# Kernel tuning notes

Hardware: AMD Instinct MI355X
Metric: run time of the kernel (lower is better)

## Reference

```python
import jax, jax.numpy as jnp
import numpy as np

N_NODES = 10000
N_GRAPHS = 64
NEG_SLOPE = 0.2
EPS = 1e-16


def gat_conv(x, src, dst, W, a_src, a_dst, bias, heads, out_ch, num_nodes):
    """PyG GATConv (shared lin, add_self_loops already applied to src/dst)."""
    xl = (x @ W).reshape(num_nodes, heads, out_ch)          # [N,H,C]
    alpha_s = jnp.einsum('nhc,hc->nh', xl, a_src)           # [N,H]
    alpha_d = jnp.einsum('nhc,hc->nh', xl, a_dst)           # [N,H]
    e = jax.nn.leaky_relu(alpha_s[src] + alpha_d[dst], NEG_SLOPE)  # [E,H]
    # segment softmax over incoming edges of each destination node
    emax = jax.ops.segment_max(e, dst, num_segments=num_nodes)
    emax = jnp.where(jnp.isfinite(emax), emax, 0.0)
    ee = jnp.exp(e - emax[dst])
    denom = jax.ops.segment_sum(ee, dst, num_segments=num_nodes)
    alpha = ee / (denom[dst] + EPS)                         # [E,H]
    msg = xl[src] * alpha[:, :, None]                       # [E,H,C]
    out = jax.ops.segment_sum(msg, dst, num_segments=num_nodes)  # [N,H,C]
    return out.reshape(num_nodes, heads * out_ch) + bias


def setup_inputs() -> dict:
    key = jax.random.key(0)
    ks = jax.random.split(key, 16)
    H, C, IN = 8, 128, 128
    x = jax.random.normal(ks[0], (N_NODES, IN), jnp.float32)
    edge_index = jax.random.randint(ks[1], (2, 320000), 0, N_NODES, jnp.int64)
    batch = jnp.sort(jax.random.randint(ks[2], (N_NODES,), 0, N_GRAPHS, jnp.int64))
    g = lambda k, shp, fan: jax.random.normal(k, shp, jnp.float32) * (1.0 / np.sqrt(fan))
    return {
        'x': x, 'edge_index': edge_index, 'batch': batch,
        'W1': g(ks[3], (IN, H * C), IN),
        'a_src1': g(ks[4], (H, C), C), 'a_dst1': g(ks[5], (H, C), C),
        'b1': jnp.zeros((H * C,), jnp.float32),
        'W2': g(ks[6], (H * C, C), H * C),
        'a_src2': g(ks[7], (1, C), C), 'a_dst2': g(ks[8], (1, C), C),
        'b2': jnp.zeros((C,), jnp.float32),
        'lin1_w': g(ks[9], (C, 128), C), 'lin1_b': jnp.zeros((128,), jnp.float32),
        'lin2_w': g(ks[10], (128, 1), 128), 'lin2_b': jnp.zeros((1,), jnp.float32),
    }


def reference(x, edge_index, batch, W1, a_src1, a_dst1, b1, W2, a_src2, a_dst2, b2,
              lin1_w, lin1_b, lin2_w, lin2_b):
    loops = jnp.arange(N_NODES, dtype=edge_index.dtype)
    src = jnp.concatenate([edge_index[0], loops])
    dst = jnp.concatenate([edge_index[1], loops])
    h = jax.nn.elu(gat_conv(x, src, dst, W1, a_src1, a_dst1, b1, 8, 128, N_NODES))
    h = jax.nn.elu(gat_conv(h, src, dst, W2, a_src2, a_dst2, b2, 1, 128, N_NODES))
    # global mean pool over graphs
    sums = jax.ops.segment_sum(h, batch, num_segments=N_GRAPHS)
    cnts = jax.ops.segment_sum(jnp.ones((N_NODES,), h.dtype), batch, num_segments=N_GRAPHS)
    pooled = sums / jnp.maximum(cnts, 1.0)[:, None]         # [G,128]
    z = jax.nn.relu(pooled @ lin1_w + lin1_b)
    return (z @ lin2_w + lin2_b).squeeze(1)                 # [G]
```

## Files before the change

### kernel.cpp

```cpp
#include <hip/hip_runtime.h>
#include <math.h>

#define N_NODES 10000
#define N_GRAPHS 64
#define E_RAW 320000
#define E_ALL (E_RAW + N_NODES)
#define NEG_SLOPE 0.2f
#define EPS 1e-16f
#define CAP 192

typedef unsigned short ushort_t;
typedef short short8 __attribute__((ext_vector_type(8)));
typedef float floatx4 __attribute__((ext_vector_type(4)));

static __device__ __forceinline__ float bfl(unsigned u) {
  union { unsigned u; float f; } v; v.u = u << 16; return v.f;
}
static __device__ __forceinline__ float bfh(unsigned u) {
  union { unsigned u; float f; } v; v.u = u & 0xFFFF0000u; return v.f;
}
static __device__ __forceinline__ ushort_t f2bf(float f) {
  union { float f; unsigned u; } v; v.f = f;
  unsigned r = v.u + 0x7FFFu + ((v.u >> 16) & 1u);
  return (ushort_t)(r >> 16);
}

static __device__ __forceinline__ void load16_lds(const ushort_t* gp, ushort_t* ldsbase, int lane) {
#if __has_builtin(__builtin_amdgcn_global_load_lds)
  __builtin_amdgcn_global_load_lds((const __attribute__((address_space(1))) void*)gp,
                                   (__attribute__((address_space(3))) void*)ldsbase, 16, 0, 0);
#else
  *(uint4*)(ldsbase + lane * 8) = *(const uint4*)gp;
#endif
}

static __device__ __forceinline__ void swz_one(const float* __restrict__ W,
                                               ushort_t* __restrict__ Wsw,
                                               int idx, int K, int N) {
  int NT = N >> 4;
  int lane = idx & 63, tile = idx >> 6;
  int nt = tile % NT, kt = tile / NT;
  int n = nt * 16 + (lane & 15);
  int kb = kt * 32 + (lane >> 4) * 8;
  ushort4 lo, hi;
  lo.x = f2bf(W[(size_t)(kb + 0) * N + n]); lo.y = f2bf(W[(size_t)(kb + 1) * N + n]);
  lo.z = f2bf(W[(size_t)(kb + 2) * N + n]); lo.w = f2bf(W[(size_t)(kb + 3) * N + n]);
  hi.x = f2bf(W[(size_t)(kb + 4) * N + n]); hi.y = f2bf(W[(size_t)(kb + 5) * N + n]);
  hi.z = f2bf(W[(size_t)(kb + 6) * N + n]); hi.w = f2bf(W[(size_t)(kb + 7) * N + n]);
  *(ushort4*)(Wsw + (size_t)idx * 8) = lo;
  *(ushort4*)(Wsw + (size_t)idx * 8 + 4) = hi;
}

__global__ __launch_bounds__(1024) void prep_k(const float* __restrict__ x,
                                               const int* __restrict__ batch,
                                               const float* __restrict__ W1,
                                               const float* __restrict__ W2,
                                               ushort_t* __restrict__ xb,
                                               ushort_t* __restrict__ W1sw,
                                               ushort_t* __restrict__ W2sw,
                                               float* __restrict__ zero0,
                                               int* __restrict__ poolcnt) {
  __shared__ int shm[N_GRAPHS];
  const int b = blockIdx.x, t = threadIdx.x;
  if (b < 49) {
    int i4 = b * 1024 + t;
    if (i4 < 49548) *(float4*)(zero0 + i4 * 4) = make_float4(0.f, 0.f, 0.f, 0.f);
  } else if (b == 49) {
    if (t < N_GRAPHS) shm[t] = 0;
    __syncthreads();
    for (int n = t; n < N_NODES; n += 1024) atomicAdd(&shm[batch[n]], 1);
    __syncthreads();
    if (t < N_GRAPHS) poolcnt[t] = shm[t];
  } else if (b < 363) {
    int i4 = (b - 50) * 1024 + t;
    if (i4 < 320000) {
      float4 v = *(const float4*)(x + (size_t)i4 * 4);
      ushort4 o;
      o.x = f2bf(v.x); o.y = f2bf(v.y); o.z = f2bf(v.z); o.w = f2bf(v.w);
      *(ushort4*)(xb + (size_t)i4 * 4) = o;
    }
  } else if (b < 379) {
    int idx = (b - 363) * 1024 + t;
    if (idx < 16384) swz_one(W1, W1sw, idx, 128, 1024);
  } else {
    int idx = (b - 379) * 1024 + t;
    if (idx < 16384) swz_one(W2, W2sw, idx, 1024, 128);
  }
}

__global__ __launch_bounds__(256) void g1f_k(const ushort_t* __restrict__ A,
                                             const ushort_t* __restrict__ Bsw,
                                             ushort_t* __restrict__ Cb,
                                             const float* __restrict__ aS,
                                             const float* __restrict__ aD,
                                             float* __restrict__ asO,
                                             float* __restrict__ adO,
                                             const int* __restrict__ ei,
                                             int* __restrict__ degc,
                                             int* __restrict__ csr) {
  __shared__ ushort_t Albuf[32 * 512];
  __shared__ float epi[4][16][68];
  const int bid = blockIdx.x, t = threadIdx.x;
  if (bid >= 632) {
    int e = (bid - 632) * 256 + t;
    if (e < E_ALL) {
      int s, d;
      if (e < E_RAW) { s = ei[e]; d = ei[E_RAW + e]; }
      else           { s = d = e - E_RAW; }
      int pos = atomicAdd(&degc[d], 1);
      if (pos < CAP) csr[d * CAP + pos] = s;
    }
    return;
  }
  const int M = N_NODES, K = 128, NT = 64;
  const int lane = t & 63, w = t >> 6;
  const int wm = w >> 1, wn = w & 1;
  const int m0 = (bid >> 3) * 128;
  const int n0 = (bid & 7) * 128;
  const int g = lane >> 4, l16 = lane & 15;

  #pragma unroll
  for (int i = 0; i < 8; i++) {
    int tile = w * 8 + i;
    int mtl = tile >> 2, kt = tile & 3;
    int r = m0 + mtl * 16 + l16; r = r < M ? r : M - 1;
    load16_lds(A + (size_t)r * K + kt * 32 + g * 8, &Albuf[tile * 512], lane);
  }
  __syncthreads();

  floatx4 acc[4][4] = {};
  #pragma unroll
  for (int kt = 0; kt < 4; kt++) {
    short8 a[4], b[4];
    #pragma unroll
    for (int mi = 0; mi < 4; mi++)
      a[mi] = *(const short8*)&Albuf[(((wm * 4 + mi) * 4 + kt) * 64 + lane) * 8];
    #pragma unroll
    for (int ni = 0; ni < 4; ni++) {
      int nt = (n0 >> 4) + wn * 4 + ni;
      b[ni] = *(const short8*)(Bsw + ((size_t)(kt * NT + nt) * 64 + lane) * 8);
    }
    #pragma unroll
    for (int mi = 0; mi < 4; mi++)
      #pragma unroll
      for (int ni = 0; ni < 4; ni++)
        acc[mi][ni] = __builtin_amdgcn_mfma_f32_16x16x32_bf16(a[mi], b[ni], acc[mi][ni], 0, 0, 0);
  }

  const int h = bid & 7;
  const int r = lane >> 2, c0 = (lane & 3) * 16;
  const int colh = wn * 64 + c0;
  float asc[16], adc[16];
  #pragma unroll
  for (int c = 0; c < 16; c++) { asc[c] = aS[h * 128 + colh + c]; adc[c] = aD[h * 128 + colh + c]; }
  #pragma unroll
  for (int mi = 0; mi < 4; mi++) {
    #pragma unroll
    for (int ni = 0; ni < 4; ni++)
      #pragma unroll
      for (int reg = 0; reg < 4; reg++)
        epi[w][g * 4 + reg][ni * 16 + l16] = acc[mi][ni][reg];
    float4 v0 = *(float4*)&epi[w][r][c0];
    float4 v1 = *(float4*)&epi[w][r][c0 + 4];
    float4 v2 = *(float4*)&epi[w][r][c0 + 8];
    float4 v3 = *(float4*)&epi[w][r][c0 + 12];
    float vr[16] = {v0.x,v0.y,v0.z,v0.w, v1.x,v1.y,v1.z,v1.w,
                    v2.x,v2.y,v2.z,v2.w, v3.x,v3.y,v3.z,v3.w};
    int grow = m0 + wm * 64 + mi * 16 + r;
    float sp = 0.f, dp = 0.f;
    ushort_t hv[16];
    #pragma unroll
    for (int c = 0; c < 16; c++) {
      sp = fmaf(vr[c], asc[c], sp);
      dp = fmaf(vr[c], adc[c], dp);
      hv[c] = f2bf(vr[c]);
    }
    sp += __shfl_xor(sp, 1); sp += __shfl_xor(sp, 2);
    dp += __shfl_xor(dp, 1); dp += __shfl_xor(dp, 2);
    if (grow < M) {
      uint4 u0, u1;
      u0.x = (unsigned)hv[0] | ((unsigned)hv[1] << 16);
      u0.y = (unsigned)hv[2] | ((unsigned)hv[3] << 16);
      u0.z = (unsigned)hv[4] | ((unsigned)hv[5] << 16);
      u0.w = (unsigned)hv[6] | ((unsigned)hv[7] << 16);
      u1.x = (unsigned)hv[8] | ((unsigned)hv[9] << 16);
      u1.y = (unsigned)hv[10] | ((unsigned)hv[11] << 16);
      u1.z = (unsigned)hv[12] | ((unsigned)hv[13] << 16);
      u1.w = (unsigned)hv[14] | ((unsigned)hv[15] << 16);
      ushort_t* cp = Cb + (size_t)grow * 1024 + (bid & 7) * 128 + wn * 64 + c0;
      *(uint4*)cp = u0;
      *(uint4*)(cp + 8) = u1;
      if ((lane & 3) == 0) {
        atomicAdd(&asO[grow * 8 + h], sp);
        atomicAdd(&adO[grow * 8 + h], dp);
      }
    }
  }
}

__global__ __launch_bounds__(256) void gemm2_k(const ushort_t* __restrict__ A,
                                               const ushort_t* __restrict__ Bsw,
                                               ushort_t* __restrict__ Cb,
                                               const float* __restrict__ aS,
                                               const float* __restrict__ aD,
                                               float* __restrict__ asO,
                                               float* __restrict__ adO) {
  const int M = N_NODES, K = 1024, NT = 8;
  __shared__ ushort_t Albuf[8 * 512];
  __shared__ float epi[4][16][68];
  const int t = threadIdx.x, lane = t & 63, w = t >> 6;
  const int wm = w >> 1, wn = w & 1;
  const int mb0 = blockIdx.x * 32;
  const int g = lane >> 4, l16 = lane & 15;

  floatx4 acc[4] = {};
  for (int ch = 0; ch < 8; ch++) {
    #pragma unroll
    for (int i = 0; i < 2; i++) {
      int tile = w * 2 + i;
      int mtl = tile >> 2, kt = tile & 3;
      int r = mb0 + mtl * 16 + l16; r = r < M ? r : M - 1;
      load16_lds(A + (size_t)r * K + (ch * 4 + kt) * 32 + g * 8, &Albuf[tile * 512], lane);
    }
    __syncthreads();
    #pragma unroll
    for (int ks = 0; ks < 4; ks++) {
      short8 a = *(const short8*)&Albuf[(((wm * 4 + ks)) * 64 + lane) * 8];
      #pragma unroll
      for (int ni = 0; ni < 4; ni++) {
        int nt = wn * 4 + ni, ktg = ch * 4 + ks;
        short8 b = *(const short8*)(Bsw + ((size_t)(ktg * NT + nt) * 64 + lane) * 8);
        acc[ni] = __builtin_amdgcn_mfma_f32_16x16x32_bf16(a, b, acc[ni], 0, 0, 0);
      }
    }
    __syncthreads();
  }

  const int r = lane >> 2, c0 = (lane & 3) * 16;
  const int colh = wn * 64 + c0;
  float asc[16], adc[16];
  #pragma unroll
  for (int c = 0; c < 16; c++) { asc[c] = aS[colh + c]; adc[c] = aD[colh + c]; }
  #pragma unroll
  for (int ni = 0; ni < 4; ni++)
    #pragma unroll
    for (int reg = 0; reg < 4; reg++)
      epi[w][g * 4 + reg][ni * 16 + l16] = acc[ni][reg];
  float4 v0 = *(float4*)&epi[w][r][c0];
  float4 v1 = *(float4*)&epi[w][r][c0 + 4];
  float4 v2 = *(float4*)&epi[w][r][c0 + 8];
  float4 v3 = *(float4*)&epi[w][r][c0 + 12];
  float vr[16] = {v0.x,v0.y,v0.z,v0.w, v1.x,v1.y,v1.z,v1.w,
                  v2.x,v2.y,v2.z,v2.w, v3.x,v3.y,v3.z,v3.w};
  int grow = mb0 + wm * 16 + r;
  float sp = 0.f, dp = 0.f;
  ushort_t hv[16];
  #pragma unroll
  for (int c = 0; c < 16; c++) {
    sp = fmaf(vr[c], asc[c], sp);
    dp = fmaf(vr[c], adc[c], dp);
    hv[c] = f2bf(vr[c]);
  }
  sp += __shfl_xor(sp, 1); sp += __shfl_xor(sp, 2);
  dp += __shfl_xor(dp, 1); dp += __shfl_xor(dp, 2);
  if (grow < M) {
    uint4 u0, u1;
    u0.x = (unsigned)hv[0] | ((unsigned)hv[1] << 16);
    u0.y = (unsigned)hv[2] | ((unsigned)hv[3] << 16);
    u0.z = (unsigned)hv[4] | ((unsigned)hv[5] << 16);
    u0.w = (unsigned)hv[6] | ((unsigned)hv[7] << 16);
    u1.x = (unsigned)hv[8] | ((unsigned)hv[9] << 16);
    u1.y = (unsigned)hv[10] | ((unsigned)hv[11] << 16);
    u1.z = (unsigned)hv[12] | ((unsigned)hv[13] << 16);
    u1.w = (unsigned)hv[14] | ((unsigned)hv[15] << 16);
    ushort_t* cp = Cb + (size_t)grow * 128 + colh;
    *(uint4*)cp = u0;
    *(uint4*)(cp + 8) = u1;
    if ((lane & 3) == 0) {
      atomicAdd(&asO[grow], sp);
      atomicAdd(&adO[grow], dp);
    }
  }
}

__global__ __launch_bounds__(64) void agg1_k(const ushort_t* __restrict__ xlb,
                                             const float* __restrict__ as1,
                                             const float* __restrict__ ad1,
                                             const float* __restrict__ b1,
                                             const int* __restrict__ degc,
                                             const int* __restrict__ csr,
                                             ushort_t* __restrict__ out) {
  const int bid = blockIdx.x, t = threadIdx.x;
  const int h = bid & 7, dst = bid >> 3;
  int deg = degc[dst]; deg = deg < CAP ? deg : CAP;
  const int beg = dst * CAP;
  __shared__ uint2 pr[CAP];
  float adh = ad1[dst * 8 + h];
  if (deg <= 64) {
    bool act = t < deg;
    int s = act ? csr[beg + t] : 0;
    float lg = -1e30f;
    if (act) {
      float v = as1[s * 8 + h] + adh;
      lg = v > 0.f ? v : NEG_SLOPE * v;
    }
    float pm = lg;
    #pragma unroll
    for (int off = 32; off; off >>= 1) pm = fmaxf(pm, __shfl_xor(pm, off));
    float ex = act ? __expf(lg - pm) : 0.f;
    float ps = ex;
    #pragma unroll
    for (int off = 32; off; off >>= 1) ps += __shfl_xor(ps, off);
    float inv = 1.0f / (ps + EPS);
    if (act) pr[t] = make_uint2((unsigned)(s * 2048), __float_as_uint(ex * inv));
    __syncthreads();
  } else {
    __shared__ int ssg[CAP];
    __shared__ float alg[CAP];
    for (int e = t; e < deg; e += 64) ssg[e] = csr[beg + e];
    __syncthreads();
    float pm = -1e30f;
    for (int e = t; e < deg; e += 64) {
      float v = as1[ssg[e] * 8 + h] + adh;
      v = v > 0.f ? v : NEG_SLOPE * v;
      alg[e] = v;
      pm = fmaxf(pm, v);
    }
    #pragma unroll
    for (int off = 32; off; off >>= 1) pm = fmaxf(pm, __shfl_xor(pm, off));
    __syncthreads();
    float ps = 0.f;
    for (int e = t; e < deg; e += 64) ps += __expf(alg[e] - pm);
    #pragma unroll
    for (int off = 32; off; off >>= 1) ps += __shfl_xor(ps, off);
    float inv = 1.0f / (ps + EPS);
    for (int e = t; e < deg; e += 64)
      pr[e] = make_uint2((unsigned)(ssg[e] * 2048), __float_as_uint(__expf(alg[e] - pm) * inv));
    __syncthreads();
  }
  const char* xbase = (const char*)xlb;
  const unsigned toff = (unsigned)(h * 256 + 4 * t);
  float acc0 = 0.f, acc1 = 0.f;
  #pragma unroll 4
  for (int e = 0; e < deg; e++) {
    uint2 p = pr[e];
    unsigned u = *(const unsigned*)(xbase + (p.x + toff));
    float a = __uint_as_float(p.y);
    acc0 = fmaf(a, bfl(u), acc0);
    acc1 = fmaf(a, bfh(u), acc1);
  }
  int o = h * 128 + 2 * t;
  float v0 = acc0 + b1[o];
  float v1 = acc1 + b1[o + 1];
  v0 = v0 > 0.f ? v0 : (__expf(v0) - 1.0f);
  v1 = v1 > 0.f ? v1 : (__expf(v1) - 1.0f);
  unsigned up = (unsigned)f2bf(v0) | ((unsigned)f2bf(v1) << 16);
  *(unsigned*)(out + (size_t)dst * 1024 + o) = up;
}

__global__ __launch_bounds__(64) void agg2_k(const ushort_t* __restrict__ xlb2,
                                             const float* __restrict__ as2,
                                             const float* __restrict__ ad2,
                                             const float* __restrict__ b2,
                                             const int* __restrict__ degc,
                                             const int* __restrict__ csr,
                                             const int* __restrict__ batch,
                                             float* __restrict__ poolsum) {
  int dst = blockIdx.x, t = threadIdx.x;
  int deg = degc[dst]; deg = deg < CAP ? deg : CAP;
  int beg = dst * CAP;
  float adv = ad2[dst];
  __shared__ uint2 pr[CAP];
  if (deg <= 64) {
    bool act = t < deg;
    int s = act ? csr[beg + t] : 0;
    float lg = -1e30f;
    if (act) {
      float v = as2[s] + adv;
      lg = v > 0.f ? v : NEG_SLOPE * v;
    }
    float pm = lg;
    #pragma unroll
    for (int off = 32; off; off >>= 1) pm = fmaxf(pm, __shfl_xor(pm, off));
    float ex = act ? __expf(lg - pm) : 0.f;
    float ps = ex;
    #pragma unroll
    for (int off = 32; off; off >>= 1) ps += __shfl_xor(ps, off);
    float inv = 1.0f / (ps + EPS);
    if (act) pr[t] = make_uint2((unsigned)(s * 256), __float_as_uint(ex * inv));
    __syncthreads();
  } else {
    __shared__ int ssg[CAP];
    __shared__ float alg[CAP];
    for (int e = t; e < deg; e += 64) ssg[e] = csr[beg + e];
    __syncthreads();
    float pm = -1e30f;
    for (int e = t; e < deg; e += 64) {
      float v = as2[ssg[e]] + adv;
      v = v > 0.f ? v : NEG_SLOPE * v;
      alg[e] = v;
      pm = fmaxf(pm, v);
    }
    #pragma unroll
    for (int off = 32; off; off >>= 1) pm = fmaxf(pm, __shfl_xor(pm, off));
    __syncthreads();
    float ps = 0.f;
    for (int e = t; e < deg; e += 64) ps += __expf(alg[e] - pm);
    #pragma unroll
    for (int off = 32; off; off >>= 1) ps += __shfl_xor(ps, off);
    float inv = 1.0f / (ps + EPS);
    for (int e = t; e < deg; e += 64)
      pr[e] = make_uint2((unsigned)(ssg[e] * 256), __float_as_uint(__expf(alg[e] - pm) * inv));
    __syncthreads();
  }
  const char* xbase = (const char*)xlb2;
  const unsigned toff = (unsigned)(4 * t);
  float acc0 = 0.f, acc1 = 0.f;
  #pragma unroll 4
  for (int e = 0; e < deg; e++) {
    uint2 p = pr[e];
    unsigned u = *(const unsigned*)(xbase + (p.x + toff));
    float a = __uint_as_float(p.y);
    acc0 = fmaf(a, bfl(u), acc0);
    acc1 = fmaf(a, bfh(u), acc1);
  }
  int c0 = 2 * t;
  float v0 = acc0 + b2[c0];
  float v1 = acc1 + b2[c0 + 1];
  v0 = v0 > 0.f ? v0 : (__expf(v0) - 1.0f);
  v1 = v1 > 0.f ? v1 : (__expf(v1) - 1.0f);
  int g = batch[dst];
  atomicAdd(&poolsum[g * 128 + c0], v0);
  atomicAdd(&poolsum[g * 128 + c0 + 1], v1);
}

__global__ __launch_bounds__(128) void final_k(const float* __restrict__ poolsum,
                                               const int* __restrict__ cnt,
                                               const float* __restrict__ l1w,
                                               const float* __restrict__ l1b,
                                               const float* __restrict__ l2w,
                                               const float* __restrict__ l2b,
                                               float* __restrict__ out) {
  int g = blockIdx.x, t = threadIdx.x;
  __shared__ float pooled[128];
  float c = fmaxf((float)cnt[g], 1.0f);
  pooled[t] = poolsum[g * 128 + t] / c;
  __syncthreads();
  float acc = l1b[t];
  for (int i = 0; i < 128; i++) acc = fmaf(pooled[i], l1w[i * 128 + t], acc);
  acc = fmaxf(acc, 0.0f);
  float p = acc * l2w[t];
  #pragma unroll
  for (int off = 32; off; off >>= 1) p += __shfl_down(p, off);
  __shared__ float r[2];
  if ((t & 63) == 0) r[t >> 6] = p;
  __syncthreads();
  if (t == 0) out[g] = r[0] + r[1] + l2b[0];
}

extern "C" void kernel_launch(void* const* d_in, const int* in_sizes, int n_in,
                              void* d_out, int out_size, void* d_ws, size_t ws_size,
                              hipStream_t stream) {
  const float* x    = (const float*)d_in[0];
  const int*   ei   = (const int*)d_in[1];
  const int*   batch= (const int*)d_in[2];
  const float* W1   = (const float*)d_in[3];
  const float* aS1  = (const float*)d_in[4];
  const float* aD1  = (const float*)d_in[5];
  const float* b1   = (const float*)d_in[6];
  const float* W2   = (const float*)d_in[7];
  const float* aS2  = (const float*)d_in[8];
  const float* aD2  = (const float*)d_in[9];
  const float* b2   = (const float*)d_in[10];
  const float* l1w  = (const float*)d_in[11];
  const float* l1b  = (const float*)d_in[12];
  const float* l2w  = (const float*)d_in[13];
  const float* l2b  = (const float*)d_in[14];
  float* out = (float*)d_out;

  ushort_t* xlb1   = (ushort_t*)d_ws;
  ushort_t* h1b    = xlb1 + 10240000;
  ushort_t* xlb2   = h1b + 10240000;
  ushort_t* xb     = xlb2 + 1280000;
  ushort_t* W1sw   = xb + 1280000;
  ushort_t* W2sw   = W1sw + 131072;
  float*    zero0  = (float*)(W2sw + 131072);
  float*    as1    = zero0;
  float*    ad1    = as1 + 80000;
  float*    as2    = ad1 + 80000;
  float*    ad2    = as2 + 10000;
  float*    poolsum= ad2 + 10000;
  int*      degc   = (int*)(poolsum + 8192);
  int*      poolcnt= degc + 10000;
  int*      csr    = poolcnt + 64;

  prep_k<<<395, 1024, 0, stream>>>(x, batch, W1, W2, xb, W1sw, W2sw, zero0, poolcnt);
  g1f_k<<<632 + 1290, 256, 0, stream>>>(xb, W1sw, xlb1, aS1, aD1, as1, ad1, ei, degc, csr);
  agg1_k<<<N_NODES * 8, 64, 0, stream>>>(xlb1, as1, ad1, b1, degc, csr, h1b);
  gemm2_k<<<313, 256, 0, stream>>>(h1b, W2sw, xlb2, aS2, aD2, as2, ad2);
  agg2_k<<<N_NODES, 64, 0, stream>>>(xlb2, as2, ad2, b2, degc, csr, batch, poolsum);
  final_k<<<N_GRAPHS, 128, 0, stream>>>(poolsum, poolcnt, l1w, l1b, l2w, l2b, out);
}
```

Measured before the change: 225.9 us.

## Pad edge lists to multiples of eight and fuse final MLP into agg2 via last-block counter

The gather loops in both aggregation kernels now run over edge lists padded to a multiple of eight with zero-weight entries. They use eight-way unrolling with four independent accumulator pairs, which gives more loads in flight and shorter FMA dependency chains. The final_k launch is removed: each agg2 block increments a per-graph completion counter, and the last block for a graph computes the pooled MLP. This saves a kernel launch but adds atomics and fences to every block. Padded entries gather node 0 with zero weight, and the zero-init range is widened to cover the new counters.

```diff
diff --git a/kernel.cpp b/kernel.cpp
--- a/kernel.cpp
+++ b/kernel.cpp
@@ -64,7 +64,7 @@
   const int b = blockIdx.x, t = threadIdx.x;
   if (b < 49) {
     int i4 = b * 1024 + t;
-    if (i4 < 49548) *(float4*)(zero0 + i4 * 4) = make_float4(0.f, 0.f, 0.f, 0.f);
+    if (i4 < 49564) *(float4*)(zero0 + i4 * 4) = make_float4(0.f, 0.f, 0.f, 0.f);
   } else if (b == 49) {
     if (t < N_GRAPHS) shm[t] = 0;
     __syncthreads();
@@ -294,6 +294,7 @@
   const int h = bid & 7, dst = bid >> 3;
   int deg = degc[dst]; deg = deg < CAP ? deg : CAP;
   const int beg = dst * CAP;
+  const int degp = (deg + 7) & ~7;
   __shared__ uint2 pr[CAP];
   float adh = ad1[dst * 8 + h];
   if (deg <= 64) {
@@ -312,7 +313,8 @@
     #pragma unroll
     for (int off = 32; off; off >>= 1) ps += __shfl_xor(ps, off);
     float inv = 1.0f / (ps + EPS);
-    if (act) pr[t] = make_uint2((unsigned)(s * 2048), __float_as_uint(ex * inv));
+    if (t < degp) pr[t] = act ? make_uint2((unsigned)(s * 2048), __float_as_uint(ex * inv))
+                              : make_uint2(0u, 0u);
     __syncthreads();
   } else {
     __shared__ int ssg[CAP];
@@ -336,19 +338,24 @@
     float inv = 1.0f / (ps + EPS);
     for (int e = t; e < deg; e += 64)
       pr[e] = make_uint2((unsigned)(ssg[e] * 2048), __float_as_uint(__expf(alg[e] - pm) * inv));
+    for (int e = deg + t; e < degp; e += 64) pr[e] = make_uint2(0u, 0u);
     __syncthreads();
   }
   const char* xbase = (const char*)xlb;
   const unsigned toff = (unsigned)(h * 256 + 4 * t);
-  float acc0 = 0.f, acc1 = 0.f;
-  #pragma unroll 4
-  for (int e = 0; e < deg; e++) {
-    uint2 p = pr[e];
-    unsigned u = *(const unsigned*)(xbase + (p.x + toff));
-    float a = __uint_as_float(p.y);
-    acc0 = fmaf(a, bfl(u), acc0);
-    acc1 = fmaf(a, bfh(u), acc1);
-  }
+  float accA[4] = {}, accB[4] = {};
+  for (int e0 = 0; e0 < degp; e0 += 8) {
+    #pragma unroll
+    for (int j = 0; j < 8; j++) {
+      uint2 p = pr[e0 + j];
+      unsigned u = *(const unsigned*)(xbase + (p.x + toff));
+      float a = __uint_as_float(p.y);
+      accA[j & 3] = fmaf(a, bfl(u), accA[j & 3]);
+      accB[j & 3] = fmaf(a, bfh(u), accB[j & 3]);
+    }
+  }
+  float acc0 = (accA[0] + accA[1]) + (accA[2] + accA[3]);
+  float acc1 = (accB[0] + accB[1]) + (accB[2] + accB[3]);
   int o = h * 128 + 2 * t;
   float v0 = acc0 + b1[o];
   float v1 = acc1 + b1[o + 1];
@@ -358,17 +365,25 @@
   *(unsigned*)(out + (size_t)dst * 1024 + o) = up;
 }
 
-__global__ __launch_bounds__(64) void agg2_k(const ushort_t* __restrict__ xlb2,
-                                             const float* __restrict__ as2,
-                                             const float* __restrict__ ad2,
-                                             const float* __restrict__ b2,
-                                             const int* __restrict__ degc,
-                                             const int* __restrict__ csr,
-                                             const int* __restrict__ batch,
-                                             float* __restrict__ poolsum) {
+__global__ __launch_bounds__(64) void agg2f_k(const ushort_t* __restrict__ xlb2,
+                                              const float* __restrict__ as2,
+                                              const float* __restrict__ ad2,
+                                              const float* __restrict__ b2,
+                                              const int* __restrict__ degc,
+                                              const int* __restrict__ csr,
+                                              const int* __restrict__ batch,
+                                              float* __restrict__ poolsum,
+                                              const int* __restrict__ poolcnt,
+                                              int* __restrict__ gdone,
+                                              const float* __restrict__ l1w,
+                                              const float* __restrict__ l1b,
+                                              const float* __restrict__ l2w,
+                                              const float* __restrict__ l2b,
+                                              float* __restrict__ out) {
   int dst = blockIdx.x, t = threadIdx.x;
   int deg = degc[dst]; deg = deg < CAP ? deg : CAP;
   int beg = dst * CAP;
+  const int degp = (deg + 7) & ~7;
   float adv = ad2[dst];
   __shared__ uint2 pr[CAP];
   if (deg <= 64) {
@@ -387,7 +402,8 @@
     #pragma unroll
     for (int off = 32; off; off >>= 1) ps += __shfl_xor(ps, off);
     float inv = 1.0f / (ps + EPS);
-    if (act) pr[t] = make_uint2((unsigned)(s * 256), __float_as_uint(ex * inv));
+    if (t < degp) pr[t] = act ? make_uint2((unsigned)(s * 256), __float_as_uint(ex * inv))
+                              : make_uint2(0u, 0u);
     __syncthreads();
   } else {
     __shared__ int ssg[CAP];
@@ -411,19 +427,24 @@
     float inv = 1.0f / (ps + EPS);
     for (int e = t; e < deg; e += 64)
       pr[e] = make_uint2((unsigned)(ssg[e] * 256), __float_as_uint(__expf(alg[e] - pm) * inv));
+    for (int e = deg + t; e < degp; e += 64) pr[e] = make_uint2(0u, 0u);
     __syncthreads();
   }
   const char* xbase = (const char*)xlb2;
   const unsigned toff = (unsigned)(4 * t);
-  float acc0 = 0.f, acc1 = 0.f;
-  #pragma unroll 4
-  for (int e = 0; e < deg; e++) {
-    uint2 p = pr[e];
-    unsigned u = *(const unsigned*)(xbase + (p.x + toff));
-    float a = __uint_as_float(p.y);
-    acc0 = fmaf(a, bfl(u), acc0);
-    acc1 = fmaf(a, bfh(u), acc1);
-  }
+  float accA[4] = {}, accB[4] = {};
+  for (int e0 = 0; e0 < degp; e0 += 8) {
+    #pragma unroll
+    for (int j = 0; j < 8; j++) {
+      uint2 p = pr[e0 + j];
+      unsigned u = *(const unsigned*)(xbase + (p.x + toff));
+      float a = __uint_as_float(p.y);
+      accA[j & 3] = fmaf(a, bfl(u), accA[j & 3]);
+      accB[j & 3] = fmaf(a, bfh(u), accB[j & 3]);
+    }
+  }
+  float acc0 = (accA[0] + accA[1]) + (accA[2] + accA[3]);
+  float acc1 = (accB[0] + accB[1]) + (accB[2] + accB[3]);
   int c0 = 2 * t;
   float v0 = acc0 + b2[c0];
   float v1 = acc1 + b2[c0 + 1];
@@ -432,30 +453,32 @@
   int g = batch[dst];
   atomicAdd(&poolsum[g * 128 + c0], v0);
   atomicAdd(&poolsum[g * 128 + c0 + 1], v1);
-}
-
-__global__ __launch_bounds__(128) void final_k(const float* __restrict__ poolsum,
-                                               const int* __restrict__ cnt,
-                                               const float* __restrict__ l1w,
-                                               const float* __restrict__ l1b,
-                                               const float* __restrict__ l2w,
-                                               const float* __restrict__ l2b,
-                                               float* __restrict__ out) {
-  int g = blockIdx.x, t = threadIdx.x;
+  int cnt = poolcnt[g];
+  __threadfence();
+  __syncthreads();
+  int lastf = 0;
+  if (t == 0) {
+    int old = __hip_atomic_fetch_add(&gdone[g], 1, __ATOMIC_ACQ_REL, __HIP_MEMORY_SCOPE_AGENT);
+    lastf = (old == cnt - 1);
+  }
+  lastf = __shfl(lastf, 0);
+  if (!lastf) return;
   __shared__ float pooled[128];
-  float c = fmaxf((float)cnt[g], 1.0f);
-  pooled[t] = poolsum[g * 128 + t] / c;
+  float c = fmaxf((float)cnt, 1.0f);
+  pooled[t]      = __hip_atomic_load(&poolsum[g * 128 + t],      __ATOMIC_ACQUIRE, __HIP_MEMORY_SCOPE_AGENT) / c;
+  pooled[t + 64] = __hip_atomic_load(&poolsum[g * 128 + t + 64], __ATOMIC_ACQUIRE, __HIP_MEMORY_SCOPE_AGENT) / c;
   __syncthreads();
-  float acc = l1b[t];
-  for (int i = 0; i < 128; i++) acc = fmaf(pooled[i], l1w[i * 128 + t], acc);
-  acc = fmaxf(acc, 0.0f);
-  float p = acc * l2w[t];
-  #pragma unroll
-  for (int off = 32; off; off >>= 1) p += __shfl_down(p, off);
-  __shared__ float r[2];
-  if ((t & 63) == 0) r[t >> 6] = p;
-  __syncthreads();
-  if (t == 0) out[g] = r[0] + r[1] + l2b[0];
+  float a0 = l1b[t], a1 = l1b[t + 64];
+  for (int i = 0; i < 128; i++) {
+    float p = pooled[i];
+    a0 = fmaf(p, l1w[i * 128 + t], a0);
+    a1 = fmaf(p, l1w[i * 128 + t + 64], a1);
+  }
+  a0 = fmaxf(a0, 0.0f); a1 = fmaxf(a1, 0.0f);
+  float s = a0 * l2w[t] + a1 * l2w[t + 64];
+  #pragma unroll
+  for (int off = 32; off; off >>= 1) s += __shfl_xor(s, off);
+  if (t == 0) out[g] = s + l2b[0];
 }
 
 extern "C" void kernel_launch(void* const* d_in, const int* in_sizes, int n_in,
@@ -491,13 +514,14 @@
   float*    ad2    = as2 + 10000;
   float*    poolsum= ad2 + 10000;
   int*      degc   = (int*)(poolsum + 8192);
-  int*      poolcnt= degc + 10000;
+  int*      gdone  = degc + 10000;
+  int*      poolcnt= gdone + 64;
   int*      csr    = poolcnt + 64;
 
   prep_k<<<395, 1024, 0, stream>>>(x, batch, W1, W2, xb, W1sw, W2sw, zero0, poolcnt);
   g1f_k<<<632 + 1290, 256, 0, stream>>>(xb, W1sw, xlb1, aS1, aD1, as1, ad1, ei, degc, csr);
   agg1_k<<<N_NODES * 8, 64, 0, stream>>>(xlb1, as1, ad1, b1, degc, csr, h1b);
   gemm2_k<<<313, 256, 0, stream>>>(h1b, W2sw, xlb2, aS2, aD2, as2, ad2);
-  agg2_k<<<N_NODES, 64, 0, stream>>>(xlb2, as2, ad2, b2, degc, csr, batch, poolsum);
-  final_k<<<N_GRAPHS, 128, 0, stream>>>(poolsum, poolcnt, l1w, l1b, l2w, l2b, out);
-}
+  agg2f_k<<<N_NODES, 64, 0, stream>>>(xlb2, as2, ad2, b2, degc, csr, batch,
+                                      poolsum, poolcnt, gdone, l1w, l1b, l2w, l2b, out);
+}
```

Result: slower. 520.4 us (+130.4%).
